# Kernel optimization log

Measured on AMD Instinct MI355X. Metric: run time of the kernel, lower is better.

The kernel has to match this reference:

```python
import jax, jax.numpy as jnp
import numpy as np

B, S = 2, 2048
H = 16
NOPE, ROPE, VD = 128, 64, 128
Q_RANK, KV_RANK = 1536, 512
SCALE = 1.0 / np.sqrt(NOPE + ROPE)  # 1/sqrt(192)
NEG_INF = -10000.0


def _make_rope(n_pos, dim):
    # matches gen_rope: theta over even indices, angles repeated twice (rotate-half layout)
    theta = 1.0 / (10000.0 ** (np.arange(0, dim, 2, dtype=np.float32) / dim))
    pos = np.arange(n_pos, dtype=np.float32)
    ang = np.outer(pos, theta)                      # [N, dim/2]
    ang = np.concatenate([ang, ang], axis=-1)       # [N, dim]
    return jnp.asarray(np.cos(ang)), jnp.asarray(np.sin(ang))


def _rope(x, cos, sin):
    # rotate-half RoPE; cos/sin broadcast over head dim if present
    d = x.shape[-1]
    x1, x2 = x[..., : d // 2], x[..., d // 2 :]
    rot = jnp.concatenate([-x2, x1], axis=-1)
    return x * cos + rot * sin


def setup_inputs() -> dict:
    key = jax.random.key(0)
    ks = jax.random.split(key, 5)
    Q = jax.random.normal(ks[0], (B, S, Q_RANK), dtype=jnp.float32)
    KV = jax.random.normal(ks[1], (B, S, KV_RANK), dtype=jnp.float32)
    PE = jax.random.normal(ks[2], (B, S, ROPE), dtype=jnp.float32)
    WUQ = jax.random.normal(ks[3], (H * (NOPE + ROPE), Q_RANK), dtype=jnp.float32) * 0.02
    WUKV = jax.random.normal(ks[4], (H * (NOPE + VD), KV_RANK), dtype=jnp.float32) * 0.02
    cos, sin = _make_rope(B * S, ROPE)
    cos = cos.reshape(B, S, ROPE)
    sin = sin.reshape(B, S, ROPE)
    mask = jnp.triu(jnp.full((S, S), NEG_INF, dtype=jnp.float32), k=1)
    return {"Q": Q, "KV": KV, "PE": PE, "WUQ": WUQ, "WUKV": WUKV,
            "cos": cos, "sin": sin, "mask": mask}


def reference(Q, KV, PE, WUQ, WUKV, cos, sin, mask):
    b, s, _ = Q.shape
    # low-rank up-projections
    q = jnp.einsum("bsl,dl->bsd", Q, WUQ).reshape(b, s, H, NOPE + ROPE)
    q_nope, q_pe = q[..., :NOPE], q[..., NOPE:]
    q_pe = _rope(q_pe, cos[:, :, None, :], sin[:, :, None, :])

    kv = jnp.einsum("bsl,dl->bsd", KV, WUKV).reshape(b, s, H, NOPE + VD)
    k_nope, v = kv[..., :NOPE], kv[..., NOPE:]
    k_pe = _rope(PE, cos, sin)  # [b, s, ROPE], shared across heads

    # attention scores: per-head nope part + shared rope part
    scores = jnp.einsum("bqhd,bkhd->bhqk", q_nope, k_nope)
    scores = scores + jnp.einsum("bqhd,bkd->bhqk", q_pe, k_pe)
    scores = scores * SCALE + mask[None, None, :, :]
    attn = jax.nn.softmax(scores, axis=-1)
    out = jnp.einsum("bhqk,bkhd->bqhd", attn, v)  # [b, s, H, VD]
    return out
```

## Files before the change

kernel.cpp:

```cpp
#include <hip/hip_runtime.h>

typedef __attribute__((ext_vector_type(8))) short short8;
typedef __attribute__((ext_vector_type(4))) float f32x4;

#define SS 2048
#define HH 16
#define NOPE_D 128
#define ROPE_D 64
#define VDIM 128
#define QD 192
#define SCALE_F 0.07216878364870323f
#define LOG2E 1.4426950408889634f

__device__ __forceinline__ unsigned short f2bf(float f) {
    unsigned int x = __builtin_bit_cast(unsigned int, f);
    unsigned int r = (x + 0x7fffu + ((x >> 16) & 1u)) >> 16;
    return (unsigned short)r;
}

#define GLDS16(g, l) __builtin_amdgcn_global_load_lds( \
    (const __attribute__((address_space(1))) void*)(g), \
    (__attribute__((address_space(3))) void*)(l), 16, 0, 0)

__global__ __launch_bounds__(256) void cvt_all(
    const float* __restrict__ Q, const float* __restrict__ WUQ,
    const float* __restrict__ KV, const float* __restrict__ WUKV,
    const float* __restrict__ PE, const float* __restrict__ cs, const float* __restrict__ sn,
    unsigned short* __restrict__ Qb, unsigned short* __restrict__ WUQb,
    unsigned short* __restrict__ KVb, unsigned short* __restrict__ WUKVb,
    unsigned short* __restrict__ kpe)
{
    int bid = blockIdx.x;
    if (bid >= 14848) {
        int idx = (bid - 14848) * 256 + threadIdx.x;
        int i = idx & 31, row = idx >> 5;
        float x1 = PE[row * 64 + i], x2 = PE[row * 64 + 32 + i];
        float c1 = cs[row * 64 + i],      s1 = sn[row * 64 + i];
        float c2 = cs[row * 64 + 32 + i], s2 = sn[row * 64 + 32 + i];
        kpe[row * 64 + i]      = f2bf(x1 * c1 - x2 * s1);
        kpe[row * 64 + 32 + i] = f2bf(x2 * c2 + x1 * s2);
        return;
    }
    const float* src; unsigned short* dst; float scale = 1.0f;
    if (bid < 6144)       { src = Q;    dst = Qb; }
    else if (bid < 10752) { src = WUQ;  dst = WUQb; bid -= 6144; scale = SCALE_F * LOG2E; }
    else if (bid < 12800) { src = KV;   dst = KVb;  bid -= 10752; }
    else                  { src = WUKV; dst = WUKVb; bid -= 12800; }
    int i = (bid * 256 + threadIdx.x) * 4;
    float4 v = *(const float4*)(src + i);
    ushort4 o = { f2bf(v.x * scale), f2bf(v.y * scale), f2bf(v.z * scale), f2bf(v.w * scale) };
    *(ushort4*)(dst + i) = o;
}

__global__ __launch_bounds__(256) void gemm_fused(
    const unsigned short* __restrict__ Qb, const unsigned short* __restrict__ WUQb,
    const unsigned short* __restrict__ KVb, const unsigned short* __restrict__ WUKVb,
    unsigned short* __restrict__ qbuf, unsigned short* __restrict__ knope,
    unsigned short* __restrict__ vT,
    const float* __restrict__ cs, const float* __restrict__ sn)
{
    __shared__ unsigned short As[128 * 64];
    __shared__ unsigned short Bs[128 * 64];
    const int t = threadIdx.x, w = t >> 6, lane = t & 63;
    const int n16 = lane & 15, quad = lane >> 4;

    int bid = blockIdx.x;
    const unsigned short *A, *B; int N, K, bm, bn; bool g1;
    if (bid < 768) { g1 = true;  A = Qb;  B = WUQb;  N = 3072; K = 1536;
                     bm = (bid / 24) * 128; bn = (bid % 24) * 128; }
    else           { g1 = false; bid -= 768; A = KVb; B = WUKVb; N = 4096; K = 512;
                     bm = (bid / 32) * 128; bn = (bid % 32) * 128; }

    const int wm = (w >> 1) * 64, wn = (w & 1) * 64;
    f32x4 acc[4][4] = {};

    const int lr = lane >> 3, lc = lane & 7;
    const int sw = (lc ^ lr) * 8;
    const unsigned short* gA = A + (size_t)(bm + w * 32 + lr) * K + sw;
    const unsigned short* gB = B + (size_t)(bn + w * 32 + lr) * K + sw;

    for (int k0 = 0; k0 < K; k0 += 64) {
        __syncthreads();
        for (int j = 0; j < 4; j++) {
            GLDS16(gA + (size_t)j * 8 * K + k0, &As[(w * 32 + j * 8) * 64]);
            GLDS16(gB + (size_t)j * 8 * K + k0, &Bs[(w * 32 + j * 8) * 64]);
        }
        __syncthreads();
        for (int ks = 0; ks < 2; ks++) {
            short8 af[4], bf[4];
            for (int mt = 0; mt < 4; mt++) {
                int rw = wm + mt * 16 + n16;
                af[mt] = *(const short8*)&As[rw * 64 + (((ks * 4 + quad) ^ (rw & 7)) * 8)];
            }
            for (int nt = 0; nt < 4; nt++) {
                int rw = wn + nt * 16 + n16;
                bf[nt] = *(const short8*)&Bs[rw * 64 + (((ks * 4 + quad) ^ (rw & 7)) * 8)];
            }
            for (int mt = 0; mt < 4; mt++)
                for (int nt = 0; nt < 4; nt++)
                    acc[mt][nt] = __builtin_amdgcn_mfma_f32_16x16x32_bf16(af[mt], bf[nt], acc[mt][nt], 0, 0, 0);
        }
    }

    const int colbase = bn + wn;
    if (g1) {
        const bool is_pe = ((colbase % 192) >= 128);
        if (is_pe) {
            for (int mt = 0; mt < 4; mt++)
                for (int r = 0; r < 4; r++) {
                    int row = bm + wm + mt * 16 + quad * 4 + r;
                    const float* cr = cs + row * 64;
                    const float* sr = sn + row * 64;
                    for (int nt = 0; nt < 2; nt++) {
                        int i = nt * 16 + n16;
                        float x1 = acc[mt][nt][r], x2 = acc[mt][nt + 2][r];
                        float o1 = x1 * cr[i] - x2 * sr[i];
                        float o2 = x2 * cr[32 + i] + x1 * sr[32 + i];
                        qbuf[(size_t)row * N + colbase + i] = f2bf(o1);
                        qbuf[(size_t)row * N + colbase + 32 + i] = f2bf(o2);
                    }
                }
        } else {
            for (int mt = 0; mt < 4; mt++)
                for (int nt = 0; nt < 4; nt++)
                    for (int r = 0; r < 4; r++)
                        qbuf[(size_t)(bm + wm + mt * 16 + quad * 4 + r) * N + colbase + nt * 16 + n16]
                            = f2bf(acc[mt][nt][r]);
        }
    } else {
        if ((colbase & 255) < 128) {
            for (int mt = 0; mt < 4; mt++)
                for (int nt = 0; nt < 4; nt++) {
                    int col = colbase + nt * 16 + n16;
                    int h = col >> 8, d = col & 255;
                    for (int r = 0; r < 4; r++)
                        knope[(size_t)(bm + wm + mt * 16 + quad * 4 + r) * 2048 + h * 128 + d]
                            = f2bf(acc[mt][nt][r]);
                }
        } else {
            for (int mt = 0; mt < 4; mt++)
                for (int nt = 0; nt < 4; nt++) {
                    int col = colbase + nt * 16 + n16;
                    int h = col >> 8, vd = (col & 255) - 128;
                    int row0 = bm + wm + mt * 16 + quad * 4;
                    int b = row0 >> 11, s0 = row0 & 2047;
                    int l6 = s0 & 63;
                    int scol = (s0 & ~63) + ((l6 >> 5) & 1) * 32 + ((l6 >> 2) & 3) * 8
                             + ((l6 >> 4) & 1) * 4 + (l6 & 3);
                    ushort4 pk = { f2bf(acc[mt][nt][0]), f2bf(acc[mt][nt][1]),
                                   f2bf(acc[mt][nt][2]), f2bf(acc[mt][nt][3]) };
                    *(ushort4*)&vT[((size_t)(b * 16 + h) * 128 + vd) * 2048 + scol] = pk;
                }
        }
    }
}

__global__ __launch_bounds__(256, 2) void attn_kernel(
    const unsigned short* __restrict__ qbuf,
    const unsigned short* __restrict__ knope,
    const unsigned short* __restrict__ kpe,
    const unsigned short* __restrict__ vT,
    float* __restrict__ out)
{
    const int t = threadIdx.x, w = t >> 6, lane = t & 63;
    const int n16 = lane & 15, quad = lane >> 4;

    __shared__ unsigned short Kn[64 * 128];
    __shared__ unsigned short Kp[64 * 64];
    __shared__ unsigned short Vt[128 * 64];
    __shared__ float Al[4][32];

    const int u = blockIdx.x;
    const int sbits = (u >> 1) & 15;
    const int flip  = (u & 1) ^ ((u >> 8) & 1);
    const int qt = flip ? 15 - sbits : sbits;
    const int c  = ((u >> 5) & 7) | ((u & 1) << 3) | (((u >> 8) & 1) << 4);
    const int h = c & 15, b = c >> 4;

    const unsigned short* knb = knope + (size_t)b * 2048 * 2048 + h * 128;
    const unsigned short* kpb = kpe + (size_t)b * 2048 * 64;
    const unsigned short* vtb = vT + (size_t)(b * 16 + h) * 128 * 2048;

    short8 qf[2][6];
    for (int qg = 0; qg < 2; qg++) {
        size_t grow = (size_t)(b * SS + qt * 128 + w * 32 + qg * 16 + n16);
        const unsigned short* qp = qbuf + grow * (HH * QD) + h * QD + quad * 8;
        for (int ks = 0; ks < 6; ks++) qf[qg][ks] = *(const short8*)(qp + ks * 32);
    }

    f32x4 O[2][8] = {};
    float m_i[2] = { -INFINITY, -INFINITY };
    float l_i[2] = { 0.f, 0.f };

    const int nkt = 2 * qt + 2;
    for (int kt = 0; kt < nkt; kt++) {
        __syncthreads();
        {
            int r = w * 16 + (lane >> 4);
            int sl = lane & 15;
            for (int j = 0; j < 4; j++) {
                int rr = r + j * 4;
                const unsigned short* g = knb + (size_t)(kt * 64 + rr) * 2048 + ((sl ^ (rr & 7)) * 8);
                GLDS16(g, &Kn[(w * 16 + j * 4) * 128]);
            }
        }
        {
            int r = w * 16 + (lane >> 3);
            int sl = lane & 7;
            for (int j = 0; j < 2; j++) {
                int rr = r + j * 8;
                const unsigned short* g = kpb + (size_t)(kt * 64 + rr) * 64 + ((sl ^ (rr & 7)) * 8);
                GLDS16(g, &Kp[(w * 16 + j * 8) * 64]);
            }
        }
        {
            int r = w * 32 + (lane >> 3);
            int sl = lane & 7;
            for (int j = 0; j < 4; j++) {
                int rr = r + j * 8;
                const unsigned short* g = vtb + (size_t)rr * 2048 + kt * 64 + ((sl ^ (rr & 7)) * 8);
                GLDS16(g, &Vt[(w * 32 + j * 8) * 64]);
            }
        }
        __syncthreads();

        f32x4 Sg[2][4];
        for (int nt = 0; nt < 4; nt++) {
            int key = nt * 16 + n16, kx = key & 7;
            f32x4 a0 = {}, a1 = {};
            for (int ks = 0; ks < 4; ks++) {
                short8 af = *(const short8*)&Kn[key * 128 + (((ks * 4 + quad) ^ kx) * 8)];
                a0 = __builtin_amdgcn_mfma_f32_16x16x32_bf16(af, qf[0][ks], a0, 0, 0, 0);
                a1 = __builtin_amdgcn_mfma_f32_16x16x32_bf16(af, qf[1][ks], a1, 0, 0, 0);
            }
            for (int ks = 0; ks < 2; ks++) {
                short8 af = *(const short8*)&Kp[key * 64 + (((ks * 4 + quad) ^ kx) * 8)];
                a0 = __builtin_amdgcn_mfma_f32_16x16x32_bf16(af, qf[0][4 + ks], a0, 0, 0, 0);
                a1 = __builtin_amdgcn_mfma_f32_16x16x32_bf16(af, qf[1][4 + ks], a1, 0, 0, 0);
            }
            Sg[0][nt] = a0; Sg[1][nt] = a1;
        }

        if (kt >= 2 * qt) {
            for (int qg = 0; qg < 2; qg++) {
                int qq = qt * 128 + w * 32 + qg * 16 + n16;
                for (int nt = 0; nt < 4; nt++) {
                    int key0 = kt * 64 + nt * 16 + quad * 4;
                    for (int r = 0; r < 4; r++)
                        if (key0 + r > qq) Sg[qg][nt][r] = -INFINITY;
                }
            }
        }

        float alpha[2];
        bool skipq[2];
        for (int qg = 0; qg < 2; qg++) {
            float mx = -INFINITY;
            for (int nt = 0; nt < 4; nt++)
                for (int r = 0; r < 4; r++) mx = fmaxf(mx, Sg[qg][nt][r]);
            mx = fmaxf(mx, __shfl_xor(mx, 16, 64));
            mx = fmaxf(mx, __shfl_xor(mx, 32, 64));
            const bool skip = __all(mx - m_i[qg] <= 8.0f);
            skipq[qg] = skip;
            float mnew = skip ? m_i[qg] : fmaxf(m_i[qg], mx);
            alpha[qg] = skip ? 1.0f : exp2f(m_i[qg] - mnew);
            m_i[qg] = mnew;
            float rs = 0.f;
            for (int nt = 0; nt < 4; nt++)
                for (int r = 0; r < 4; r++) {
                    float pv = exp2f(Sg[qg][nt][r] - mnew);
                    Sg[qg][nt][r] = pv;
                    rs += pv;
                }
            l_i[qg] = l_i[qg] * alpha[qg] + rs;
        }
        if (quad == 0) { Al[w][n16] = alpha[0]; Al[w][16 + n16] = alpha[1]; }
        if (!skipq[0]) {
            f32x4 av0 = *(const f32x4*)&Al[w][quad * 4];
            for (int v8 = 0; v8 < 8; v8++)
                for (int r = 0; r < 4; r++) O[0][v8][r] *= av0[r];
        }
        if (!skipq[1]) {
            f32x4 av1 = *(const f32x4*)&Al[w][16 + quad * 4];
            for (int v8 = 0; v8 < 8; v8++)
                for (int r = 0; r < 4; r++) O[1][v8][r] *= av1[r];
        }

        short8 pp[2][2];
        for (int qg = 0; qg < 2; qg++)
            for (int ntp = 0; ntp < 2; ntp++) {
                short8 pa;
                for (int j = 0; j < 4; j++) pa[j] = (short)f2bf(Sg[qg][ntp * 2][j]);
                for (int j = 0; j < 4; j++) pa[4 + j] = (short)f2bf(Sg[qg][ntp * 2 + 1][j]);
                pp[qg][ntp] = pa;
            }
        for (int ntp = 0; ntp < 2; ntp++)
            for (int v8 = 0; v8 < 8; v8++) {
                int vd = v8 * 16 + n16;
                short8 vb = *(const short8*)&Vt[vd * 64 + (((ntp * 4 + quad) ^ (vd & 7)) * 8)];
                O[0][v8] = __builtin_amdgcn_mfma_f32_16x16x32_bf16(pp[0][ntp], vb, O[0][v8], 0, 0, 0);
                O[1][v8] = __builtin_amdgcn_mfma_f32_16x16x32_bf16(pp[1][ntp], vb, O[1][v8], 0, 0, 0);
            }
    }

    {
        float l0 = l_i[0];
        l0 += __shfl_xor(l0, 16, 64); l0 += __shfl_xor(l0, 32, 64);
        float l1 = l_i[1];
        l1 += __shfl_xor(l1, 16, 64); l1 += __shfl_xor(l1, 32, 64);
        if (quad == 0) { Al[w][n16] = 1.f / l0; Al[w][16 + n16] = 1.f / l1; }
    }
    f32x4 lv0 = *(const f32x4*)&Al[w][quad * 4];
    f32x4 lv1 = *(const f32x4*)&Al[w][16 + quad * 4];
    for (int qg = 0; qg < 2; qg++) {
        const f32x4 lv = qg ? lv1 : lv0;
        for (int r = 0; r < 4; r++) {
            size_t qrow = (size_t)(b * SS + qt * 128 + w * 32 + qg * 16 + quad * 4 + r);
            float* op = out + (qrow * HH + h) * VDIM;
            for (int v8 = 0; v8 < 8; v8++)
                op[v8 * 16 + n16] = O[qg][v8][r] * lv[r];
        }
    }
}

extern "C" void kernel_launch(void* const* d_in, const int* in_sizes, int n_in,
                              void* d_out, int out_size, void* d_ws, size_t ws_size,
                              hipStream_t stream) {
    const float* Q    = (const float*)d_in[0];
    const float* KV   = (const float*)d_in[1];
    const float* PE   = (const float*)d_in[2];
    const float* WUQ  = (const float*)d_in[3];
    const float* WUKV = (const float*)d_in[4];
    const float* cosp = (const float*)d_in[5];
    const float* sinp = (const float*)d_in[6];
    float* out = (float*)d_out;

    unsigned short* qbuf  = (unsigned short*)d_ws;
    unsigned short* knope = qbuf  + (size_t)4096 * 3072;
    unsigned short* vT    = knope + (size_t)4096 * 2048;
    unsigned short* kpe   = vT    + (size_t)4096 * 2048;
    unsigned short* Qb    = kpe   + (size_t)4096 * 64;
    unsigned short* WUQb  = Qb    + (size_t)4096 * 1536;
    unsigned short* KVb   = WUQb  + (size_t)3072 * 1536;
    unsigned short* WUKVb = KVb   + (size_t)4096 * 512;

    cvt_all<<<15360, 256, 0, stream>>>(Q, WUQ, KV, WUKV, PE, cosp, sinp,
                                       Qb, WUQb, KVb, WUKVb, kpe);
    gemm_fused<<<1792, 256, 0, stream>>>(Qb, WUQb, KVb, WUKVb,
                                         qbuf, knope, vT, cosp, sinp);
    attn_kernel<<<512, 256, 0, stream>>>(qbuf, knope, kpe, vT, out);
}
```

Before: 286.2 us.

## Read K, K-rope and V tiles directly from global memory instead of LDS

Removes LDS staging of the K-nope, K-pe and V-transposed tiles and the two block barriers per key tile. Each wave now loads its MFMA operands straight from global memory. This drops barrier and LDS traffic, but the four waves no longer share a tile, so each one re-reads the same K/V data from global memory and L2. The loads are also strided rows with 16-byte accesses, which can increase memory latency and request count.

```diff
diff --git a/kernel.cpp b/kernel.cpp
--- a/kernel.cpp
+++ b/kernel.cpp
@@ -165,9 +165,6 @@
     const int t = threadIdx.x, w = t >> 6, lane = t & 63;
     const int n16 = lane & 15, quad = lane >> 4;
 
-    __shared__ unsigned short Kn[64 * 128];
-    __shared__ unsigned short Kp[64 * 64];
-    __shared__ unsigned short Vt[128 * 64];
     __shared__ float Al[4][32];
 
     const int u = blockIdx.x;
@@ -194,47 +191,21 @@
 
     const int nkt = 2 * qt + 2;
     for (int kt = 0; kt < nkt; kt++) {
-        __syncthreads();
-        {
-            int r = w * 16 + (lane >> 4);
-            int sl = lane & 15;
-            for (int j = 0; j < 4; j++) {
-                int rr = r + j * 4;
-                const unsigned short* g = knb + (size_t)(kt * 64 + rr) * 2048 + ((sl ^ (rr & 7)) * 8);
-                GLDS16(g, &Kn[(w * 16 + j * 4) * 128]);
-            }
-        }
-        {
-            int r = w * 16 + (lane >> 3);
-            int sl = lane & 7;
-            for (int j = 0; j < 2; j++) {
-                int rr = r + j * 8;
-                const unsigned short* g = kpb + (size_t)(kt * 64 + rr) * 64 + ((sl ^ (rr & 7)) * 8);
-                GLDS16(g, &Kp[(w * 16 + j * 8) * 64]);
-            }
-        }
-        {
-            int r = w * 32 + (lane >> 3);
-            int sl = lane & 7;
-            for (int j = 0; j < 4; j++) {
-                int rr = r + j * 8;
-                const unsigned short* g = vtb + (size_t)rr * 2048 + kt * 64 + ((sl ^ (rr & 7)) * 8);
-                GLDS16(g, &Vt[(w * 32 + j * 8) * 64]);
-            }
-        }
-        __syncthreads();
+        const unsigned short* kb  = knb + (size_t)kt * 64 * 2048;
+        const unsigned short* kpp = kpb + (size_t)kt * 64 * 64;
+        const unsigned short* vb0 = vtb + kt * 64;
 
         f32x4 Sg[2][4];
         for (int nt = 0; nt < 4; nt++) {
-            int key = nt * 16 + n16, kx = key & 7;
+            int key = nt * 16 + n16;
             f32x4 a0 = {}, a1 = {};
             for (int ks = 0; ks < 4; ks++) {
-                short8 af = *(const short8*)&Kn[key * 128 + (((ks * 4 + quad) ^ kx) * 8)];
+                short8 af = *(const short8*)(kb + (size_t)key * 2048 + (ks * 4 + quad) * 8);
                 a0 = __builtin_amdgcn_mfma_f32_16x16x32_bf16(af, qf[0][ks], a0, 0, 0, 0);
                 a1 = __builtin_amdgcn_mfma_f32_16x16x32_bf16(af, qf[1][ks], a1, 0, 0, 0);
             }
             for (int ks = 0; ks < 2; ks++) {
-                short8 af = *(const short8*)&Kp[key * 64 + (((ks * 4 + quad) ^ kx) * 8)];
+                short8 af = *(const short8*)(kpp + (size_t)key * 64 + (ks * 4 + quad) * 8);
                 a0 = __builtin_amdgcn_mfma_f32_16x16x32_bf16(af, qf[0][4 + ks], a0, 0, 0, 0);
                 a1 = __builtin_amdgcn_mfma_f32_16x16x32_bf16(af, qf[1][4 + ks], a1, 0, 0, 0);
             }
@@ -297,7 +268,7 @@
         for (int ntp = 0; ntp < 2; ntp++)
             for (int v8 = 0; v8 < 8; v8++) {
                 int vd = v8 * 16 + n16;
-                short8 vb = *(const short8*)&Vt[vd * 64 + (((ntp * 4 + quad) ^ (vd & 7)) * 8)];
+                short8 vb = *(const short8*)(vb0 + (size_t)vd * 2048 + (ntp * 4 + quad) * 8);
                 O[0][v8] = __builtin_amdgcn_mfma_f32_16x16x32_bf16(pp[0][ntp], vb, O[0][v8], 0, 0, 0);
                 O[1][v8] = __builtin_amdgcn_mfma_f32_16x16x32_bf16(pp[1][ntp], vb, O[1][v8], 0, 0, 0);
             }
```

Measured after the change: 424.6 us. 1.48x slower.

## Split causal attention KV range across paired blocks and merge partials

Applied to the files above, without the earlier changes.

Each attention block now handles two segments: the first half of the KV range for query tile qtA, and the second half for query tile 15-qtA. This gives every block roughly equal work under the causal mask. Partial outputs are stored in bf16 scratch (low half) and unnormalized fp32 in out (high half), along with the running max and sum per half. A new combine kernel then merges the two halves with log-sum-exp rescaling. The goal is to remove load imbalance and tail effects, at the cost of an extra kernel launch, extra global traffic, and bf16 rounding of the partial output.

```diff
diff --git a/kernel.cpp b/kernel.cpp
--- a/kernel.cpp
+++ b/kernel.cpp
@@ -16,6 +16,9 @@
     unsigned int x = __builtin_bit_cast(unsigned int, f);
     unsigned int r = (x + 0x7fffu + ((x >> 16) & 1u)) >> 16;
     return (unsigned short)r;
+}
+__device__ __forceinline__ float bf2f(unsigned short u) {
+    return __builtin_bit_cast(float, (unsigned int)u << 16);
 }
 
 #define GLDS16(g, l) __builtin_amdgcn_global_load_lds( \
@@ -155,12 +158,15 @@
     }
 }
 
-__global__ __launch_bounds__(256, 2) void attn_kernel(
+__global__ __launch_bounds__(256, 2) void attn_part(
     const unsigned short* __restrict__ qbuf,
     const unsigned short* __restrict__ knope,
     const unsigned short* __restrict__ kpe,
     const unsigned short* __restrict__ vT,
-    float* __restrict__ out)
+    float* __restrict__ out,
+    unsigned short* __restrict__ OloB,
+    float2* __restrict__ mlLo,
+    float2* __restrict__ mlHi)
 {
     const int t = threadIdx.x, w = t >> 6, lane = t & 63;
     const int n16 = lane & 15, quad = lane >> 4;
@@ -170,157 +176,212 @@
     __shared__ unsigned short Vt[128 * 64];
     __shared__ float Al[4][32];
 
-    const int u = blockIdx.x;
-    const int sbits = (u >> 1) & 15;
-    const int flip  = (u & 1) ^ ((u >> 8) & 1);
-    const int qt = flip ? 15 - sbits : sbits;
-    const int c  = ((u >> 5) & 7) | ((u & 1) << 3) | (((u >> 8) & 1) << 4);
-    const int h = c & 15, b = c >> 4;
+    const int j = blockIdx.x;
+    const int qtA = j >> 5, cc = j & 31;
+    const int h = cc & 15, b = cc >> 4;
 
     const unsigned short* knb = knope + (size_t)b * 2048 * 2048 + h * 128;
     const unsigned short* kpb = kpe + (size_t)b * 2048 * 64;
     const unsigned short* vtb = vT + (size_t)(b * 16 + h) * 128 * 2048;
 
-    short8 qf[2][6];
-    for (int qg = 0; qg < 2; qg++) {
-        size_t grow = (size_t)(b * SS + qt * 128 + w * 32 + qg * 16 + n16);
-        const unsigned short* qp = qbuf + grow * (HH * QD) + h * QD + quad * 8;
-        for (int ks = 0; ks < 6; ks++) qf[qg][ks] = *(const short8*)(qp + ks * 32);
-    }
-
-    f32x4 O[2][8] = {};
-    float m_i[2] = { -INFINITY, -INFINITY };
-    float l_i[2] = { 0.f, 0.f };
-
-    const int nkt = 2 * qt + 2;
-    for (int kt = 0; kt < nkt; kt++) {
-        __syncthreads();
-        {
-            int r = w * 16 + (lane >> 4);
-            int sl = lane & 15;
-            for (int j = 0; j < 4; j++) {
-                int rr = r + j * 4;
-                const unsigned short* g = knb + (size_t)(kt * 64 + rr) * 2048 + ((sl ^ (rr & 7)) * 8);
-                GLDS16(g, &Kn[(w * 16 + j * 4) * 128]);
-            }
-        }
-        {
-            int r = w * 16 + (lane >> 3);
-            int sl = lane & 7;
-            for (int j = 0; j < 2; j++) {
-                int rr = r + j * 8;
-                const unsigned short* g = kpb + (size_t)(kt * 64 + rr) * 64 + ((sl ^ (rr & 7)) * 8);
-                GLDS16(g, &Kp[(w * 16 + j * 8) * 64]);
-            }
-        }
-        {
-            int r = w * 32 + (lane >> 3);
-            int sl = lane & 7;
-            for (int j = 0; j < 4; j++) {
-                int rr = r + j * 8;
-                const unsigned short* g = vtb + (size_t)rr * 2048 + kt * 64 + ((sl ^ (rr & 7)) * 8);
-                GLDS16(g, &Vt[(w * 32 + j * 8) * 64]);
-            }
-        }
-        __syncthreads();
-
-        f32x4 Sg[2][4];
-        for (int nt = 0; nt < 4; nt++) {
-            int key = nt * 16 + n16, kx = key & 7;
-            f32x4 a0 = {}, a1 = {};
-            for (int ks = 0; ks < 4; ks++) {
-                short8 af = *(const short8*)&Kn[key * 128 + (((ks * 4 + quad) ^ kx) * 8)];
-                a0 = __builtin_amdgcn_mfma_f32_16x16x32_bf16(af, qf[0][ks], a0, 0, 0, 0);
-                a1 = __builtin_amdgcn_mfma_f32_16x16x32_bf16(af, qf[1][ks], a1, 0, 0, 0);
-            }
-            for (int ks = 0; ks < 2; ks++) {
-                short8 af = *(const short8*)&Kp[key * 64 + (((ks * 4 + quad) ^ kx) * 8)];
-                a0 = __builtin_amdgcn_mfma_f32_16x16x32_bf16(af, qf[0][4 + ks], a0, 0, 0, 0);
-                a1 = __builtin_amdgcn_mfma_f32_16x16x32_bf16(af, qf[1][4 + ks], a1, 0, 0, 0);
-            }
-            Sg[0][nt] = a0; Sg[1][nt] = a1;
-        }
-
-        if (kt >= 2 * qt) {
+    for (int seg = 0; seg < 2; ++seg) {
+        const int qt    = seg ? (15 - qtA) : qtA;
+        const int ktbeg = seg ? (qt + 1)   : 0;
+        const int ktend = seg ? (2 * qt + 2) : (qt + 1);
+        const int uid   = qt * 32 + cc;
+
+        short8 qf[2][6];
+        for (int qg = 0; qg < 2; qg++) {
+            size_t grow = (size_t)(b * SS + qt * 128 + w * 32 + qg * 16 + n16);
+            const unsigned short* qp = qbuf + grow * (HH * QD) + h * QD + quad * 8;
+            for (int ks = 0; ks < 6; ks++) qf[qg][ks] = *(const short8*)(qp + ks * 32);
+        }
+
+        f32x4 O[2][8] = {};
+        float m_i[2] = { -INFINITY, -INFINITY };
+        float l_i[2] = { 0.f, 0.f };
+
+        for (int kt = ktbeg; kt < ktend; kt++) {
+            __syncthreads();
+            {
+                int r = w * 16 + (lane >> 4);
+                int sl = lane & 15;
+                for (int jj = 0; jj < 4; jj++) {
+                    int rr = r + jj * 4;
+                    const unsigned short* g = knb + (size_t)(kt * 64 + rr) * 2048 + ((sl ^ (rr & 7)) * 8);
+                    GLDS16(g, &Kn[(w * 16 + jj * 4) * 128]);
+                }
+            }
+            {
+                int r = w * 16 + (lane >> 3);
+                int sl = lane & 7;
+                for (int jj = 0; jj < 2; jj++) {
+                    int rr = r + jj * 8;
+                    const unsigned short* g = kpb + (size_t)(kt * 64 + rr) * 64 + ((sl ^ (rr & 7)) * 8);
+                    GLDS16(g, &Kp[(w * 16 + jj * 8) * 64]);
+                }
+            }
+            {
+                int r = w * 32 + (lane >> 3);
+                int sl = lane & 7;
+                for (int jj = 0; jj < 4; jj++) {
+                    int rr = r + jj * 8;
+                    const unsigned short* g = vtb + (size_t)rr * 2048 + kt * 64 + ((sl ^ (rr & 7)) * 8);
+                    GLDS16(g, &Vt[(w * 32 + jj * 8) * 64]);
+                }
+            }
+            __syncthreads();
+
+            f32x4 Sg[2][4];
+            for (int nt = 0; nt < 4; nt++) {
+                int key = nt * 16 + n16, kx = key & 7;
+                f32x4 a0 = {}, a1 = {};
+                for (int ks = 0; ks < 4; ks++) {
+                    short8 af = *(const short8*)&Kn[key * 128 + (((ks * 4 + quad) ^ kx) * 8)];
+                    a0 = __builtin_amdgcn_mfma_f32_16x16x32_bf16(af, qf[0][ks], a0, 0, 0, 0);
+                    a1 = __builtin_amdgcn_mfma_f32_16x16x32_bf16(af, qf[1][ks], a1, 0, 0, 0);
+                }
+                for (int ks = 0; ks < 2; ks++) {
+                    short8 af = *(const short8*)&Kp[key * 64 + (((ks * 4 + quad) ^ kx) * 8)];
+                    a0 = __builtin_amdgcn_mfma_f32_16x16x32_bf16(af, qf[0][4 + ks], a0, 0, 0, 0);
+                    a1 = __builtin_amdgcn_mfma_f32_16x16x32_bf16(af, qf[1][4 + ks], a1, 0, 0, 0);
+                }
+                Sg[0][nt] = a0; Sg[1][nt] = a1;
+            }
+
+            if (kt >= 2 * qt) {
+                for (int qg = 0; qg < 2; qg++) {
+                    int qq = qt * 128 + w * 32 + qg * 16 + n16;
+                    for (int nt = 0; nt < 4; nt++) {
+                        int key0 = kt * 64 + nt * 16 + quad * 4;
+                        for (int r = 0; r < 4; r++)
+                            if (key0 + r > qq) Sg[qg][nt][r] = -INFINITY;
+                    }
+                }
+            }
+
+            float alpha[2];
+            bool skipq[2];
             for (int qg = 0; qg < 2; qg++) {
-                int qq = qt * 128 + w * 32 + qg * 16 + n16;
-                for (int nt = 0; nt < 4; nt++) {
-                    int key0 = kt * 64 + nt * 16 + quad * 4;
-                    for (int r = 0; r < 4; r++)
-                        if (key0 + r > qq) Sg[qg][nt][r] = -INFINITY;
-                }
-            }
-        }
-
-        float alpha[2];
-        bool skipq[2];
-        for (int qg = 0; qg < 2; qg++) {
-            float mx = -INFINITY;
-            for (int nt = 0; nt < 4; nt++)
-                for (int r = 0; r < 4; r++) mx = fmaxf(mx, Sg[qg][nt][r]);
-            mx = fmaxf(mx, __shfl_xor(mx, 16, 64));
-            mx = fmaxf(mx, __shfl_xor(mx, 32, 64));
-            const bool skip = __all(mx - m_i[qg] <= 8.0f);
-            skipq[qg] = skip;
-            float mnew = skip ? m_i[qg] : fmaxf(m_i[qg], mx);
-            alpha[qg] = skip ? 1.0f : exp2f(m_i[qg] - mnew);
-            m_i[qg] = mnew;
-            float rs = 0.f;
-            for (int nt = 0; nt < 4; nt++)
-                for (int r = 0; r < 4; r++) {
-                    float pv = exp2f(Sg[qg][nt][r] - mnew);
-                    Sg[qg][nt][r] = pv;
-                    rs += pv;
-                }
-            l_i[qg] = l_i[qg] * alpha[qg] + rs;
-        }
-        if (quad == 0) { Al[w][n16] = alpha[0]; Al[w][16 + n16] = alpha[1]; }
-        if (!skipq[0]) {
-            f32x4 av0 = *(const f32x4*)&Al[w][quad * 4];
-            for (int v8 = 0; v8 < 8; v8++)
-                for (int r = 0; r < 4; r++) O[0][v8][r] *= av0[r];
-        }
-        if (!skipq[1]) {
-            f32x4 av1 = *(const f32x4*)&Al[w][16 + quad * 4];
-            for (int v8 = 0; v8 < 8; v8++)
-                for (int r = 0; r < 4; r++) O[1][v8][r] *= av1[r];
-        }
-
-        short8 pp[2][2];
-        for (int qg = 0; qg < 2; qg++)
-            for (int ntp = 0; ntp < 2; ntp++) {
-                short8 pa;
-                for (int j = 0; j < 4; j++) pa[j] = (short)f2bf(Sg[qg][ntp * 2][j]);
-                for (int j = 0; j < 4; j++) pa[4 + j] = (short)f2bf(Sg[qg][ntp * 2 + 1][j]);
-                pp[qg][ntp] = pa;
-            }
-        for (int ntp = 0; ntp < 2; ntp++)
-            for (int v8 = 0; v8 < 8; v8++) {
-                int vd = v8 * 16 + n16;
-                short8 vb = *(const short8*)&Vt[vd * 64 + (((ntp * 4 + quad) ^ (vd & 7)) * 8)];
-                O[0][v8] = __builtin_amdgcn_mfma_f32_16x16x32_bf16(pp[0][ntp], vb, O[0][v8], 0, 0, 0);
-                O[1][v8] = __builtin_amdgcn_mfma_f32_16x16x32_bf16(pp[1][ntp], vb, O[1][v8], 0, 0, 0);
-            }
-    }
-
-    {
+                float mx = -INFINITY;
+                for (int nt = 0; nt < 4; nt++)
+                    for (int r = 0; r < 4; r++) mx = fmaxf(mx, Sg[qg][nt][r]);
+                mx = fmaxf(mx, __shfl_xor(mx, 16, 64));
+                mx = fmaxf(mx, __shfl_xor(mx, 32, 64));
+                const bool skip = __all(mx <= m_i[qg] + 8.0f);
+                skipq[qg] = skip;
+                float mnew = skip ? m_i[qg] : fmaxf(m_i[qg], mx);
+                alpha[qg] = skip ? 1.0f : exp2f(m_i[qg] - mnew);
+                m_i[qg] = mnew;
+                const float msub = (mnew == -INFINITY) ? 0.0f : mnew;
+                float rs = 0.f;
+                for (int nt = 0; nt < 4; nt++)
+                    for (int r = 0; r < 4; r++) {
+                        float pv = exp2f(Sg[qg][nt][r] - msub);
+                        Sg[qg][nt][r] = pv;
+                        rs += pv;
+                    }
+                l_i[qg] = l_i[qg] * alpha[qg] + rs;
+            }
+            if (quad == 0) { Al[w][n16] = alpha[0]; Al[w][16 + n16] = alpha[1]; }
+            if (!skipq[0]) {
+                f32x4 av0 = *(const f32x4*)&Al[w][quad * 4];
+                for (int v8 = 0; v8 < 8; v8++)
+                    for (int r = 0; r < 4; r++) O[0][v8][r] *= av0[r];
+            }
+            if (!skipq[1]) {
+                f32x4 av1 = *(const f32x4*)&Al[w][16 + quad * 4];
+                for (int v8 = 0; v8 < 8; v8++)
+                    for (int r = 0; r < 4; r++) O[1][v8][r] *= av1[r];
+            }
+
+            short8 pp[2][2];
+            for (int qg = 0; qg < 2; qg++)
+                for (int ntp = 0; ntp < 2; ntp++) {
+                    short8 pa;
+                    for (int jj = 0; jj < 4; jj++) pa[jj] = (short)f2bf(Sg[qg][ntp * 2][jj]);
+                    for (int jj = 0; jj < 4; jj++) pa[4 + jj] = (short)f2bf(Sg[qg][ntp * 2 + 1][jj]);
+                    pp[qg][ntp] = pa;
+                }
+            for (int ntp = 0; ntp < 2; ntp++)
+                for (int v8 = 0; v8 < 8; v8++) {
+                    int vd = v8 * 16 + n16;
+                    short8 vb = *(const short8*)&Vt[vd * 64 + (((ntp * 4 + quad) ^ (vd & 7)) * 8)];
+                    O[0][v8] = __builtin_amdgcn_mfma_f32_16x16x32_bf16(pp[0][ntp], vb, O[0][v8], 0, 0, 0);
+                    O[1][v8] = __builtin_amdgcn_mfma_f32_16x16x32_bf16(pp[1][ntp], vb, O[1][v8], 0, 0, 0);
+                }
+        }
+
         float l0 = l_i[0];
         l0 += __shfl_xor(l0, 16, 64); l0 += __shfl_xor(l0, 32, 64);
         float l1 = l_i[1];
         l1 += __shfl_xor(l1, 16, 64); l1 += __shfl_xor(l1, 32, 64);
-        if (quad == 0) { Al[w][n16] = 1.f / l0; Al[w][16 + n16] = 1.f / l1; }
+
+        if (seg == 0) {
+            unsigned short* lb = OloB + (size_t)uid * 128 * 128;
+            for (int qg = 0; qg < 2; qg++)
+                for (int r = 0; r < 4; r++) {
+                    int row = w * 32 + qg * 16 + quad * 4 + r;
+                    unsigned short* lp = lb + (size_t)row * 128;
+                    for (int v8 = 0; v8 < 8; v8++)
+                        lp[v8 * 16 + n16] = f2bf(O[qg][v8][r]);
+                }
+            if (quad == 0) {
+                mlLo[uid * 128 + w * 32 + n16]      = make_float2(m_i[0], l0);
+                mlLo[uid * 128 + w * 32 + 16 + n16] = make_float2(m_i[1], l1);
+            }
+        } else {
+            for (int qg = 0; qg < 2; qg++)
+                for (int r = 0; r < 4; r++) {
+                    size_t qrow = (size_t)(b * SS + qt * 128 + w * 32 + qg * 16 + quad * 4 + r);
+                    float* op = out + (qrow * HH + h) * VDIM;
+                    for (int v8 = 0; v8 < 8; v8++)
+                        op[v8 * 16 + n16] = O[qg][v8][r];
+                }
+            if (quad == 0) {
+                mlHi[uid * 128 + w * 32 + n16]      = make_float2(m_i[0], l0);
+                mlHi[uid * 128 + w * 32 + 16 + n16] = make_float2(m_i[1], l1);
+            }
+        }
     }
-    f32x4 lv0 = *(const f32x4*)&Al[w][quad * 4];
-    f32x4 lv1 = *(const f32x4*)&Al[w][16 + quad * 4];
-    for (int qg = 0; qg < 2; qg++) {
-        const f32x4 lv = qg ? lv1 : lv0;
-        for (int r = 0; r < 4; r++) {
-            size_t qrow = (size_t)(b * SS + qt * 128 + w * 32 + qg * 16 + quad * 4 + r);
-            float* op = out + (qrow * HH + h) * VDIM;
-            for (int v8 = 0; v8 < 8; v8++)
-                op[v8 * 16 + n16] = O[qg][v8][r] * lv[r];
-        }
-    }
+}
+
+__global__ __launch_bounds__(256) void attn_combine(
+    const unsigned short* __restrict__ OloB,
+    const float2* __restrict__ mlLo, const float2* __restrict__ mlHi,
+    float* __restrict__ out)
+{
+    int idx = blockIdx.x * 256 + threadIdx.x;
+    int vd8 = idx & 15;
+    int rowg = idx >> 4;
+    int uid = rowg >> 7, row = rowg & 127;
+    int qt = uid >> 5, cc = uid & 31, h = cc & 15, b = cc >> 4;
+
+    float2 lo = mlLo[rowg], hi = mlHi[rowg];
+    float m  = fmaxf(lo.x, hi.x);
+    float al = exp2f(lo.x - m);
+    float ah = exp2f(hi.x - m);
+    float rl = 1.f / (lo.y * al + hi.y * ah);
+    al *= rl; ah *= rl;
+
+    const unsigned short* lp = OloB + (size_t)rowg * 128 + vd8 * 8;
+    float* op = out + ((size_t)(b * SS + qt * 128 + row) * HH + h) * VDIM + vd8 * 8;
+
+    ushort4 u0 = *(const ushort4*)lp;
+    ushort4 u1 = *(const ushort4*)(lp + 4);
+    float4 h0 = *(const float4*)op;
+    float4 h1 = *(const float4*)(op + 4);
+    float4 o0, o1;
+    o0.x = bf2f(u0.x) * al + h0.x * ah;
+    o0.y = bf2f(u0.y) * al + h0.y * ah;
+    o0.z = bf2f(u0.z) * al + h0.z * ah;
+    o0.w = bf2f(u0.w) * al + h0.w * ah;
+    o1.x = bf2f(u1.x) * al + h1.x * ah;
+    o1.y = bf2f(u1.y) * al + h1.y * ah;
+    o1.z = bf2f(u1.z) * al + h1.z * ah;
+    o1.w = bf2f(u1.w) * al + h1.w * ah;
+    *(float4*)op = o0;
+    *(float4*)(op + 4) = o1;
 }
 
 extern "C" void kernel_launch(void* const* d_in, const int* in_sizes, int n_in,
@@ -344,9 +405,14 @@
     unsigned short* KVb   = WUQb  + (size_t)3072 * 1536;
     unsigned short* WUKVb = KVb   + (size_t)4096 * 512;
 
+    unsigned short* OloB = Qb;
+    float2* mlLo = (float2*)KVb;
+    float2* mlHi = (float2*)WUKVb;
+
     cvt_all<<<15360, 256, 0, stream>>>(Q, WUQ, KV, WUKV, PE, cosp, sinp,
                                        Qb, WUQb, KVb, WUKVb, kpe);
     gemm_fused<<<1792, 256, 0, stream>>>(Qb, WUQb, KVb, WUKVb,
                                          qbuf, knope, vT, cosp, sinp);
-    attn_kernel<<<512, 256, 0, stream>>>(qbuf, knope, kpe, vT, out);
-}
+    attn_part<<<512, 256, 0, stream>>>(qbuf, knope, kpe, vT, out, OloB, mlLo, mlHi);
+    attn_combine<<<4096, 256, 0, stream>>>(OloB, mlLo, mlHi, out);
+}
```

Result: faster. 280.4 us (-2.0%).
